# Optimization experiments

Hardware: AMD Instinct MI355X
Metric: run time of the kernel (lower is better)

Reference implementation:

```python
import jax, jax.numpy as jnp
import numpy as np
import math

B, N = 1, 768
C_S, C_Z, C_H, H, P_QK, P_V = 256, 128, 128, 8, 8, 12
EPS, INF, LN_EPS = 1e-8, 1e5, 1e-5


def _quat_to_rot(q):
    # q: [..., 4] normalized quaternion (w, x, y, z) -> [..., 3, 3]
    w, x, y, z = jnp.moveaxis(q, -1, 0)
    r = jnp.stack([
        1 - 2 * (y * y + z * z), 2 * (x * y - w * z), 2 * (x * z + w * y),
        2 * (x * y + w * z), 1 - 2 * (x * x + z * z), 2 * (y * z - w * x),
        2 * (x * z - w * y), 2 * (y * z + w * x), 1 - 2 * (x * x + y * y),
    ], axis=-1)
    return r.reshape(q.shape[:-1] + (3, 3))


def _ln(x, g, b):
    mu = x.mean(-1, keepdims=True)
    var = ((x - mu) ** 2).mean(-1, keepdims=True)
    return (x - mu) * jax.lax.rsqrt(var + LN_EPS) * g + b


def setup_inputs():
    key = jax.random.key(0)
    ks = jax.random.split(key, 20)
    inp = {}
    inp['s'] = jax.random.normal(ks[0], (B, N, C_S), jnp.float32)
    inp['p'] = jax.random.normal(ks[1], (B, N, N, C_Z), jnp.float32)
    q = jax.random.normal(ks[2], (B, N, 4), jnp.float32)
    inp['rot'] = _quat_to_rot(q / jnp.linalg.norm(q, axis=-1, keepdims=True))
    inp['trans'] = 10.0 * jax.random.normal(ks[3], (B, N, 3), jnp.float32)
    inp['mask'] = jnp.ones((B, N), jnp.float32)
    concat_dim = H * C_H + H * P_V * 4 + H * C_Z
    dims = {'q': (H * C_H, C_S), 'kv': (2 * H * C_H, C_S), 'qp': (H * P_QK * 3, C_S),
            'kvp': (H * (P_QK + P_V) * 3, C_S), 'pb': (H, C_Z), 'o': (C_S, concat_dim),
            't1': (C_S, C_S), 't2': (C_S, C_S), 't3': (C_S, C_S), 'bb': (6, C_S)}
    i = 4
    for nm, (do, di) in dims.items():
        k1, k2 = jax.random.split(ks[i]); i += 1
        inp['W' + nm] = 0.02 * jax.random.normal(k1, (do, di), jnp.float32)
        inp['b' + nm] = 0.02 * jax.random.normal(k2, (do,), jnp.float32)
    inp['head_w'] = 0.1 * jax.random.normal(ks[i], (H,), jnp.float32)
    inp['g1'] = jnp.ones((C_S,), jnp.float32)
    inp['be1'] = jnp.zeros((C_S,), jnp.float32)
    inp['g2'] = jnp.ones((C_S,), jnp.float32)
    inp['be2'] = jnp.zeros((C_S,), jnp.float32)
    return inp


def reference(s, p, rot, trans, mask, Wq, bq, Wkv, bkv, Wqp, bqp, Wkvp, bkvp,
              Wpb, bpb, Wo, bo, Wt1, bt1, Wt2, bt2, Wt3, bt3, Wbb, bbb,
              head_w, g1, be1, g2, be2):
    # ---------------- Invariant Point Attention ----------------
    q = (s @ Wq.T + bq).reshape(B, N, H, C_H)
    kv = (s @ Wkv.T + bkv).reshape(B, N, H, 2 * C_H)
    k, v = kv[..., :C_H], kv[..., C_H:]
    # points: linear output is coordinate-major (x-block, y-block, z-block)
    qp = (s @ Wqp.T + bqp).reshape(B, N, 3, H, P_QK)
    qp = jnp.einsum('bnij,bnjhp->bnhpi', rot, qp) + trans[:, :, None, None, :]
    kvp = (s @ Wkvp.T + bkvp).reshape(B, N, 3, H, P_QK + P_V)
    kvp = jnp.einsum('bnij,bnjhp->bnhpi', rot, kvp) + trans[:, :, None, None, :]
    kp, vp = kvp[..., :P_QK, :], kvp[..., P_QK:, :]
    bias_p = p @ Wpb.T + bpb  # [B,N,N,H]
    a = jnp.einsum('bihc,bjhc->bhij', q, k) * math.sqrt(1.0 / (3 * C_H))
    a = a + math.sqrt(1.0 / 3) * jnp.transpose(bias_p, (0, 3, 1, 2))
    d2 = ((qp[:, :, None] - kp[:, None]) ** 2).sum(-1)  # [B,N,N,H,Pqk]
    hw = jax.nn.softplus(head_w) * math.sqrt(1.0 / (3 * (P_QK * 9.0 / 2)))
    pt_att = -0.5 * (d2 * hw[None, None, None, :, None]).sum(-1)  # [B,N,N,H]
    m2 = mask[:, :, None] * mask[:, None, :]
    a = a + jnp.transpose(pt_att, (0, 3, 1, 2)) + (INF * (m2 - 1.0))[:, None]
    att = jax.nn.softmax(a, axis=-1)  # [B,H,N,N]
    o = jnp.einsum('bhij,bjhc->bihc', att, v).reshape(B, N, H * C_H)
    opt = jnp.einsum('bhij,bjhpx->bihpx', att, vp)  # [B,N,H,Pv,3] global
    opt = jnp.einsum('bnji,bnhpj->bnhpi', rot, opt - trans[:, :, None, None, :])
    opt_norm = jnp.sqrt((opt ** 2).sum(-1) + EPS).reshape(B, N, H * P_V)
    opt_flat = jnp.moveaxis(opt.reshape(B, N, H * P_V, 3), -1, -2).reshape(B, N, 3 * H * P_V)
    opair = jnp.einsum('bhij,bijz->bihz', att, p).reshape(B, N, H * C_Z)
    ipa_out = jnp.concatenate([o, opt_flat, opt_norm, opair], -1) @ Wo.T + bo
    # residual + dropout(eval: identity) + LayerNorm
    s1 = _ln(s + ipa_out, g1, be1)
    # ---------------- StructureTransition (1 layer) ----------------
    x = jax.nn.relu(s1 @ Wt1.T + bt1)
    x = jax.nn.relu(x @ Wt2.T + bt2)
    s2 = _ln(s1 + (x @ Wt3.T + bt3), g2, be2)
    # ---------------- BackboneUpdate + masked quaternion compose ----------------
    upd = (s2 @ Wbb.T + bbb) * mask[..., None]  # [B,N,6]
    qvec = jnp.concatenate([jnp.ones(upd.shape[:-1] + (1,), upd.dtype), upd[..., :3]], -1)
    qvec = qvec / jnp.linalg.norm(qvec, axis=-1, keepdims=True)
    rot_new = jnp.einsum('bnij,bnjk->bnik', rot, _quat_to_rot(qvec))
    trans_new = trans + jnp.einsum('bnij,bnj->bni', rot, upd[..., 3:])
    return (s2, rot_new, trans_new)
```

## Files before the change

kernel.cpp:

```cpp
#include <hip/hip_runtime.h>
#include <hip/hip_bf16.h>
#include <math.h>

#define NN 768
#define CS 256
#define CZ 128
#define CH 128
#define HH 8
#define PQK 8
#define PV 12
#define CONCAT 2432
#define ATT_HSTRIDE (768*768)

typedef __bf16 v8bf __attribute__((ext_vector_type(8)));
typedef __bf16 v4bf __attribute__((ext_vector_type(4)));
typedef float  v4f  __attribute__((ext_vector_type(4)));

__device__ inline unsigned short f2bf(float f) {
    union { float f; unsigned u; } v; v.f = f;
    unsigned r = v.u + 0x7FFFu + ((v.u >> 16) & 1u);
    return (unsigned short)(r >> 16);
}
__device__ inline float bf2f(unsigned short u) {
    union { unsigned u; float f; } v; v.u = ((unsigned)u) << 16; return v.f;
}
__device__ inline unsigned encf(float f) {
    unsigned u = __float_as_uint(f);
    return (u >> 31) ? ~u : (u | 0x80000000u);
}
__device__ inline float decf(unsigned e) {
    unsigned u = (e >> 31) ? (e & 0x7FFFFFFFu) : ~e;
    return __uint_as_float(u);
}
__device__ inline v8bf cvt8(const float* p) {
    float4 a = *(const float4*)p;
    float4 b = *(const float4*)(p + 4);
    v8bf v;
    v[0] = (__bf16)a.x; v[1] = (__bf16)a.y; v[2] = (__bf16)a.z; v[3] = (__bf16)a.w;
    v[4] = (__bf16)b.x; v[5] = (__bf16)b.y; v[6] = (__bf16)b.z; v[7] = (__bf16)b.w;
    return v;
}

struct ProjDesc {
    const float* W[4];
    const float* bias[4];
    unsigned short* dstb[4];
    float* dstf[4];
    int D[4];
    int ldc[4];
    int mode[4];
    int blk_start[5];
};

__global__ __launch_bounds__(256) void proj_all(const float* __restrict__ S, ProjDesc d)
{
    __shared__ unsigned short As[64][40];
    __shared__ unsigned short Ws[64][40];
    int bx = blockIdx.x;
    int seg = 0;
    #pragma unroll
    for (int q = 0; q < 3; q++) if (bx >= d.blk_start[q + 1]) seg = q + 1;
    int bd = (bx - d.blk_start[seg]) * 64;
    int bi = blockIdx.y * 64;
    const float* W = d.W[seg];
    int D = d.D[seg], ldc = d.ldc[seg];

    int tid = threadIdx.x, lane = tid & 63, wid = tid >> 6;
    int wr = (wid >> 1) * 32, wc = (wid & 1) * 32;
    v4f acc[2][2] = {};
    int lrow = tid >> 2, lcol = (tid & 3) * 8;
    const float* Ap = S + (size_t)(bi + lrow) * 256 + lcol;
    const float* Wp = W + (size_t)(bd + lrow) * 256 + lcol;
    bool wv = (bd + lrow) < D;
    int fr = lane & 15, fc = (lane >> 4) * 8;

    for (int k0 = 0; k0 < 256; k0 += 32) {
        *(v8bf*)&As[lrow][lcol] = cvt8(Ap + k0);
        v8bf wz = {};
        *(v8bf*)&Ws[lrow][lcol] = wv ? cvt8(Wp + k0) : wz;
        __syncthreads();
        v8bf a0 = *(const v8bf*)&As[wr + fr][fc];
        v8bf a1 = *(const v8bf*)&As[wr + 16 + fr][fc];
        v8bf b0 = *(const v8bf*)&Ws[wc + fr][fc];
        v8bf b1 = *(const v8bf*)&Ws[wc + 16 + fr][fc];
        acc[0][0] = __builtin_amdgcn_mfma_f32_16x16x32_bf16(a0, b0, acc[0][0], 0, 0, 0);
        acc[0][1] = __builtin_amdgcn_mfma_f32_16x16x32_bf16(a0, b1, acc[0][1], 0, 0, 0);
        acc[1][0] = __builtin_amdgcn_mfma_f32_16x16x32_bf16(a1, b0, acc[1][0], 0, 0, 0);
        acc[1][1] = __builtin_amdgcn_mfma_f32_16x16x32_bf16(a1, b1, acc[1][1], 0, 0, 0);
        __syncthreads();
    }
    const float* bias = d.bias[seg];
    int mode = d.mode[seg];
    unsigned short* Cb = d.dstb[seg];
    float* Cf = d.dstf[seg];
    int mrow = (lane >> 4) * 4;
    #pragma unroll
    for (int mi = 0; mi < 2; mi++) {
        #pragma unroll
        for (int ni = 0; ni < 2; ni++) {
            int dd = bd + wc + ni * 16 + fr;
            if (dd < D) {
                #pragma unroll
                for (int r = 0; r < 4; r++) {
                    int m = bi + wr + mi * 16 + mrow + r;
                    float v = acc[mi][ni][r] + bias[dd];
                    if (mode == 2) Cb[(size_t)m * ldc + dd] = f2bf(v);
                    else           Cf[(size_t)m * ldc + dd] = v;
                }
            }
        }
    }
}

__global__ __launch_bounds__(256) void wo_gemm(
    const unsigned short* __restrict__ A,
    const float* __restrict__ W,
    float* __restrict__ C)
{
    __shared__ unsigned short As[64][40];
    __shared__ unsigned short Ws[64][40];
    const int K = 2432, D = 256, ldc = 256;
    int tid = threadIdx.x;
    int bi = blockIdx.y * 64;
    int bd = blockIdx.x * 64;
    int kpb = K / 4;
    int k0b = blockIdx.z * kpb;
    int lane = tid & 63;
    int wid = tid >> 6;
    int wr = (wid >> 1) * 32, wc = (wid & 1) * 32;
    v4f acc[2][2] = {};
    int lrow = tid >> 2;
    int lcol = (tid & 3) * 8;
    const unsigned short* Ap = A + (size_t)(bi + lrow) * K + lcol;
    const float* Wp = W + (size_t)(bd + lrow) * K + lcol;
    int fr = lane & 15, fc = (lane >> 4) * 8;

    for (int k0 = k0b; k0 < k0b + kpb; k0 += 32) {
        *(int4*)&As[lrow][lcol] = *(const int4*)(Ap + k0);
        *(v8bf*)&Ws[lrow][lcol] = cvt8(Wp + k0);
        __syncthreads();
        v8bf a0 = *(const v8bf*)&As[wr + fr][fc];
        v8bf a1 = *(const v8bf*)&As[wr + 16 + fr][fc];
        v8bf b0 = *(const v8bf*)&Ws[wc + fr][fc];
        v8bf b1 = *(const v8bf*)&Ws[wc + 16 + fr][fc];
        acc[0][0] = __builtin_amdgcn_mfma_f32_16x16x32_bf16(a0, b0, acc[0][0], 0, 0, 0);
        acc[0][1] = __builtin_amdgcn_mfma_f32_16x16x32_bf16(a0, b1, acc[0][1], 0, 0, 0);
        acc[1][0] = __builtin_amdgcn_mfma_f32_16x16x32_bf16(a1, b0, acc[1][0], 0, 0, 0);
        acc[1][1] = __builtin_amdgcn_mfma_f32_16x16x32_bf16(a1, b1, acc[1][1], 0, 0, 0);
        __syncthreads();
    }
    int mrow = (lane >> 4) * 4;
    #pragma unroll
    for (int mi = 0; mi < 2; mi++) {
        #pragma unroll
        for (int ni = 0; ni < 2; ni++) {
            int d = bd + wc + ni * 16 + fr;
            #pragma unroll
            for (int r = 0; r < 4; r++) {
                int m = bi + wr + mi * 16 + mrow + r;
                atomicAdd(&C[(size_t)m * ldc + d], acc[mi][ni][r]);
            }
        }
    }
}

__global__ __launch_bounds__(256) void prep2_kernel(
    const float* __restrict__ qpraw, const float* __restrict__ kvpraw,
    const float* __restrict__ rot, const float* __restrict__ trans,
    const unsigned short* __restrict__ kv_bf,
    unsigned short* __restrict__ qph, unsigned short* __restrict__ qpl,
    unsigned short* __restrict__ kph, unsigned short* __restrict__ kpl,
    unsigned short* __restrict__ Vc)
{
    __shared__ unsigned short tile[32][136];
    int bx = blockIdx.x;
    int t = threadIdx.x;
    if (bx < 672) {
        int id = bx*256 + t;
        int i = id / (HH*28);
        int rem = id % (HH*28);
        int h = rem / 28;
        int idx = rem % 28;
        const float* R = rot + i*9;
        const float* T = trans + i*3;
        float s0, s1, s2;
        if (idx < 8) {
            s0 = qpraw[i*192 +   0 + h*8 + idx];
            s1 = qpraw[i*192 +  64 + h*8 + idx];
            s2 = qpraw[i*192 + 128 + h*8 + idx];
        } else {
            int pp = idx - 8;
            s0 = kvpraw[i*480 +   0 + h*20 + pp];
            s1 = kvpraw[i*480 + 160 + h*20 + pp];
            s2 = kvpraw[i*480 + 320 + h*20 + pp];
        }
        float ov[3];
        ov[0] = R[0]*s0 + R[1]*s1 + R[2]*s2 + T[0];
        ov[1] = R[3]*s0 + R[4]*s1 + R[5]*s2 + T[1];
        ov[2] = R[6]*s0 + R[7]*s1 + R[8]*s2 + T[2];
        if (idx < 8) {
            #pragma unroll
            for (int x = 0; x < 3; x++) {
                unsigned short hi = f2bf(ov[x]);
                qph[i*256 + h*32 + idx*3 + x] = hi;
                qpl[i*256 + h*32 + idx*3 + x] = f2bf(ov[x] - bf2f(hi));
            }
            if (idx == 0) {
                #pragma unroll
                for (int m = 24; m < 32; m++) { qph[i*256+h*32+m] = 0; qpl[i*256+h*32+m] = 0; }
            }
        } else if (idx < 16) {
            int pp = idx - 8;
            #pragma unroll
            for (int x = 0; x < 3; x++) {
                unsigned short hi = f2bf(ov[x]);
                kph[i*256 + h*32 + pp*3 + x] = hi;
                kpl[i*256 + h*32 + pp*3 + x] = f2bf(ov[x] - bf2f(hi));
            }
            if (idx == 8) {
                #pragma unroll
                for (int m = 24; m < 32; m++) { kph[i*256+h*32+m] = 0; kpl[i*256+h*32+m] = 0; }
            }
        } else {
            int ppv = idx - 16;
            #pragma unroll
            for (int x = 0; x < 3; x++)
                Vc[((size_t)h*192 + 128 + ppv*3 + x)*768 + i] = f2bf(ov[x]);
        }
    } else {
        int bx2 = bx - 672;
        int h = bx2 & 7, jt = bx2 >> 3;
        int r = t >> 3, c0 = (t & 7) * 16;
        const unsigned short* src = kv_bf + (size_t)(jt*32 + r)*2048 + h*256 + 128 + c0;
        *(int4*)&tile[r][c0]     = *(const int4*)src;
        *(int4*)&tile[r][c0 + 8] = *(const int4*)(src + 8);
        __syncthreads();
        int c = t >> 1, jh = (t & 1) * 16;
        unsigned short tmp[16];
        #pragma unroll
        for (int k = 0; k < 16; k++) tmp[k] = tile[jh + k][c];
        unsigned short* dst = Vc + ((size_t)h*192 + c)*768 + jt*32 + jh;
        *(int4*)dst       = *(int4*)&tmp[0];
        *(int4*)(dst + 8) = *(int4*)&tmp[8];
    }
}

__global__ __launch_bounds__(256) void logits_mfma(
    const unsigned short* __restrict__ q_bf, const unsigned short* __restrict__ kv_bf,
    const unsigned short* __restrict__ qph, const unsigned short* __restrict__ qpl,
    const unsigned short* __restrict__ kph, const unsigned short* __restrict__ kpl,
    const float* __restrict__ mask, const float* __restrict__ head_w,
    float* __restrict__ att, unsigned* __restrict__ m0enc)
{
    __shared__ unsigned short Qs[64][136];
    __shared__ unsigned short Ks[64][136];
    __shared__ float Mi[64], Mj[64];
    int h = blockIdx.z;
    int i0 = blockIdx.y * 64, j0 = blockIdx.x * 64;
    int tid = threadIdx.x, lane = tid & 63, wid = tid >> 6;
    int wr = (wid >> 1) * 32, wc = (wid & 1) * 32;
    int r = tid >> 2, cq = (tid & 3) * 32;
    const unsigned short* qg = q_bf  + (size_t)(i0 + r)*1024 + h*128 + cq;
    const unsigned short* kg = kv_bf + (size_t)(j0 + r)*2048 + h*256 + cq;
    #pragma unroll
    for (int kk = 0; kk < 4; kk++) {
        *(int4*)&Qs[r][cq + kk*8] = *(const int4*)(qg + kk*8);
        *(int4*)&Ks[r][cq + kk*8] = *(const int4*)(kg + kk*8);
    }
    if (tid < 64) {
        Mi[tid] = mask[i0 + tid];
        Mj[tid] = mask[j0 + tid];
    }
    int fr = lane & 15, fc = (lane >> 4) * 8;
    v8bf ah0 = *(const v8bf*)&qph[(size_t)(i0 + wr + fr)*256 + h*32 + fc];
    v8bf ah1 = *(const v8bf*)&qph[(size_t)(i0 + wr + 16 + fr)*256 + h*32 + fc];
    v8bf al0 = *(const v8bf*)&qpl[(size_t)(i0 + wr + fr)*256 + h*32 + fc];
    v8bf al1 = *(const v8bf*)&qpl[(size_t)(i0 + wr + 16 + fr)*256 + h*32 + fc];
    v8bf bh0 = *(const v8bf*)&kph[(size_t)(j0 + wc + fr)*256 + h*32 + fc];
    v8bf bh1 = *(const v8bf*)&kph[(size_t)(j0 + wc + 16 + fr)*256 + h*32 + fc];
    v8bf bl0 = *(const v8bf*)&kpl[(size_t)(j0 + wc + fr)*256 + h*32 + fc];
    v8bf bl1 = *(const v8bf*)&kpl[(size_t)(j0 + wc + 16 + fr)*256 + h*32 + fc];
    float q2a = 0.f, q2b = 0.f, k2a = 0.f, k2b = 0.f;
    #pragma unroll
    for (int m = 0; m < 8; m++) {
        float va = (float)ah0[m] + (float)al0[m];
        float vb = (float)ah1[m] + (float)al1[m];
        float wa = (float)bh0[m] + (float)bl0[m];
        float wb = (float)bh1[m] + (float)bl1[m];
        q2a += va*va; q2b += vb*vb; k2a += wa*wa; k2b += wb*wb;
    }
    q2a += __shfl_xor(q2a, 16); q2a += __shfl_xor(q2a, 32);
    q2b += __shfl_xor(q2b, 16); q2b += __shfl_xor(q2b, 32);
    k2a += __shfl_xor(k2a, 16); k2a += __shfl_xor(k2a, 32);
    k2b += __shfl_xor(k2b, 16); k2b += __shfl_xor(k2b, 32);

    v4f ap[2][2] = {};
    ap[0][0] = __builtin_amdgcn_mfma_f32_16x16x32_bf16(ah0, bh0, ap[0][0], 0, 0, 0);
    ap[0][1] = __builtin_amdgcn_mfma_f32_16x16x32_bf16(ah0, bh1, ap[0][1], 0, 0, 0);
    ap[1][0] = __builtin_amdgcn_mfma_f32_16x16x32_bf16(ah1, bh0, ap[1][0], 0, 0, 0);
    ap[1][1] = __builtin_amdgcn_mfma_f32_16x16x32_bf16(ah1, bh1, ap[1][1], 0, 0, 0);
    ap[0][0] = __builtin_amdgcn_mfma_f32_16x16x32_bf16(ah0, bl0, ap[0][0], 0, 0, 0);
    ap[0][1] = __builtin_amdgcn_mfma_f32_16x16x32_bf16(ah0, bl1, ap[0][1], 0, 0, 0);
    ap[1][0] = __builtin_amdgcn_mfma_f32_16x16x32_bf16(ah1, bl0, ap[1][0], 0, 0, 0);
    ap[1][1] = __builtin_amdgcn_mfma_f32_16x16x32_bf16(ah1, bl1, ap[1][1], 0, 0, 0);
    ap[0][0] = __builtin_amdgcn_mfma_f32_16x16x32_bf16(al0, bh0, ap[0][0], 0, 0, 0);
    ap[0][1] = __builtin_amdgcn_mfma_f32_16x16x32_bf16(al0, bh1, ap[0][1], 0, 0, 0);
    ap[1][0] = __builtin_amdgcn_mfma_f32_16x16x32_bf16(al1, bh0, ap[1][0], 0, 0, 0);
    ap[1][1] = __builtin_amdgcn_mfma_f32_16x16x32_bf16(al1, bh1, ap[1][1], 0, 0, 0);

    __syncthreads();
    v4f aqk[2][2] = {};
    #pragma unroll
    for (int ks = 0; ks < 4; ks++) {
        v8bf a0 = *(const v8bf*)&Qs[wr + fr][ks*32 + fc];
        v8bf a1 = *(const v8bf*)&Qs[wr + 16 + fr][ks*32 + fc];
        v8bf b0 = *(const v8bf*)&Ks[wc + fr][ks*32 + fc];
        v8bf b1 = *(const v8bf*)&Ks[wc + 16 + fr][ks*32 + fc];
        aqk[0][0] = __builtin_amdgcn_mfma_f32_16x16x32_bf16(a0, b0, aqk[0][0], 0, 0, 0);
        aqk[0][1] = __builtin_amdgcn_mfma_f32_16x16x32_bf16(a0, b1, aqk[0][1], 0, 0, 0);
        aqk[1][0] = __builtin_amdgcn_mfma_f32_16x16x32_bf16(a1, b0, aqk[1][0], 0, 0, 0);
        aqk[1][1] = __builtin_amdgcn_mfma_f32_16x16x32_bf16(a1, b1, aqk[1][1], 0, 0, 0);
    }
    float hx = head_w[h];
    float sp = (hx > 20.f) ? hx : log1pf(__expf(hx));
    float hw = sp * 0.09622504486493764f;
    const float scale_qk = 0.05103103630798288f;
    int mrow = (lane >> 4) * 4;
    float val[2][2][4];
    #pragma unroll
    for (int mi = 0; mi < 2; mi++) {
        #pragma unroll
        for (int rr = 0; rr < 4; rr++) {
            float qss = __shfl((mi == 0) ? q2a : q2b, mrow + rr);
            #pragma unroll
            for (int ni = 0; ni < 2; ni++) {
                int jl = wc + ni*16 + fr;
                int il = wr + mi*16 + mrow + rr;
                float kss = (ni == 0) ? k2a : k2b;
                float v = aqk[mi][ni][rr]*scale_qk + hw*ap[mi][ni][rr]
                        - 0.5f*hw*(qss + kss)
                        + 100000.0f*(Mi[il]*Mj[jl] - 1.0f);
                val[mi][ni][rr] = v;
                att[(size_t)h*ATT_HSTRIDE + (size_t)(i0 + il)*768 + (j0 + jl)] = v;
            }
        }
    }
    #pragma unroll
    for (int mi = 0; mi < 2; mi++) {
        #pragma unroll
        for (int rr = 0; rr < 4; rr++) {
            float m = fmaxf(val[mi][0][rr], val[mi][1][rr]);
            #pragma unroll
            for (int d2 = 1; d2 < 16; d2 <<= 1) m = fmaxf(m, __shfl_xor(m, d2));
            if (fr == 0) {
                int il = wr + mi*16 + mrow + rr;
                atomicMax(&m0enc[h*768 + i0 + il], encf(m));
            }
        }
    }
}

__global__ __launch_bounds__(256) void fused_p4_kernel(
    const float* __restrict__ att0,
    const float* __restrict__ p,
    const float* __restrict__ Wpb, const float* __restrict__ bpb,
    const unsigned* __restrict__ m0enc,
    unsigned short* __restrict__ att_bf,
    float* __restrict__ lpart,
    float* __restrict__ opart)
{
    __shared__ unsigned short ptile[2][64][132];
    __shared__ unsigned short wt[16][72];
    __shared__ float bpb_s[8], m8[8], lsum_w[4][8];

    int i = blockIdx.x;
    int quarter = blockIdx.y;
    int jbase = quarter * 192;
    int tid = threadIdx.x, lane = tid & 63, wid = tid >> 6;
    int fr = lane & 15, fc = (lane >> 4) * 8;
    int mrow = (lane >> 4) * 4;

    for (int idx = tid; idx < 16*72; idx += 256) ((unsigned short*)wt)[idx] = 0;
    if (tid < 8) {
        bpb_s[tid] = bpb[tid];
        m8[tid] = decf(m0enc[tid*768 + i]);
    }

    v8bf aW[4];
    #pragma unroll
    for (int ks = 0; ks < 4; ks++) {
        v8bf v = {};
        if (fr < 8) v = cvt8(Wpb + fr*128 + ks*32 + fc);
        aW[ks] = v;
    }

    const float* pbase = p + (size_t)i*98304 + (size_t)jbase*128;
    int ldrow = tid >> 4, ldz = (tid & 15) * 8;
    float4 pfA[4], pfB[4];
    #pragma unroll
    for (int r2 = 0; r2 < 4; r2++) {
        const float* src = pbase + (size_t)(r2*16 + ldrow)*128 + ldz;
        pfA[r2] = *(const float4*)src;
        pfB[r2] = *(const float4*)(src + 4);
    }
    #pragma unroll
    for (int r2 = 0; r2 < 4; r2++) {
        v4bf lo, hi;
        lo[0] = (__bf16)pfA[r2].x; lo[1] = (__bf16)pfA[r2].y;
        lo[2] = (__bf16)pfA[r2].z; lo[3] = (__bf16)pfA[r2].w;
        hi[0] = (__bf16)pfB[r2].x; hi[1] = (__bf16)pfB[r2].y;
        hi[2] = (__bf16)pfB[r2].z; hi[3] = (__bf16)pfB[r2].w;
        *(v4bf*)&ptile[0][r2*16 + ldrow][ldz]     = lo;
        *(v4bf*)&ptile[0][r2*16 + ldrow][ldz + 4] = hi;
    }
    #pragma unroll
    for (int r2 = 0; r2 < 4; r2++) {
        const float* src = pbase + (size_t)(64 + r2*16 + ldrow)*128 + ldz;
        pfA[r2] = *(const float4*)src;
        pfB[r2] = *(const float4*)(src + 4);
    }
    __syncthreads();
    float m0l[4];
    #pragma unroll
    for (int r2 = 0; r2 < 4; r2++) m0l[r2] = (mrow == 0) ? m8[r2] : m8[4 + r2];

    v4f accD[2] = {};
    float lacc[4] = {0.f, 0.f, 0.f, 0.f};
    const float sqrt13 = 0.57735026918962576f;
    bool expo = (mrow < 8);

    for (int t64 = 0; t64 < 3; t64++) {
        int cur = t64 & 1;
        int j0 = jbase + t64 * 64;

        v4f bd = {};
        #pragma unroll
        for (int ks = 0; ks < 4; ks++) {
            int c = ks*32 + fc;
            v4bf blo = *(const v4bf*)&ptile[cur][16*wid + fr][c];
            v4bf bhi = *(const v4bf*)&ptile[cur][16*wid + fr][c + 4];
            v8bf b;
            b[0]=blo[0]; b[1]=blo[1]; b[2]=blo[2]; b[3]=blo[3];
            b[4]=bhi[0]; b[5]=bhi[1]; b[6]=bhi[2]; b[7]=bhi[3];
            bd = __builtin_amdgcn_mfma_f32_16x16x32_bf16(aW[ks], b, bd, 0, 0, 0);
        }
        if (expo) {
            int j = 16*wid + fr;
            float a0v[4], w8[4];
            #pragma unroll
            for (int r2 = 0; r2 < 4; r2++)
                a0v[r2] = att0[((size_t)(mrow + r2)*768 + i)*768 + j0 + j];
            #pragma unroll
            for (int r2 = 0; r2 < 4; r2++) {
                int h = mrow + r2;
                float L = a0v[r2] + sqrt13*(bd[r2] + bpb_s[h]);
                w8[r2] = __expf(fminf(L - m0l[r2], 60.f));
            }
            #pragma unroll
            for (int r2 = 0; r2 < 4; r2++) {
                int h = mrow + r2;
                unsigned short wb = f2bf(w8[r2]);
                wt[h][j] = wb;
                att_bf[((size_t)h*768 + i)*768 + j0 + j] = wb;
            }
            #pragma unroll
            for (int m = 1; m < 16; m <<= 1) {
                #pragma unroll
                for (int r2 = 0; r2 < 4; r2++) w8[r2] += __shfl_xor(w8[r2], m);
            }
            #pragma unroll
            for (int r2 = 0; r2 < 4; r2++) lacc[r2] += w8[r2];
        }
        if (t64 < 2) {
            #pragma unroll
            for (int r2 = 0; r2 < 4; r2++) {
                v4bf lo, hi;
                lo[0] = (__bf16)pfA[r2].x; lo[1] = (__bf16)pfA[r2].y;
                lo[2] = (__bf16)pfA[r2].z; lo[3] = (__bf16)pfA[r2].w;
                hi[0] = (__bf16)pfB[r2].x; hi[1] = (__bf16)pfB[r2].y;
                hi[2] = (__bf16)pfB[r2].z; hi[3] = (__bf16)pfB[r2].w;
                *(v4bf*)&ptile[cur ^ 1][r2*16 + ldrow][ldz]     = lo;
                *(v4bf*)&ptile[cur ^ 1][r2*16 + ldrow][ldz + 4] = hi;
            }
            if (t64 < 1) {
                #pragma unroll
                for (int r2 = 0; r2 < 4; r2++) {
                    const float* src = pbase + (size_t)((t64+2)*64 + r2*16 + ldrow)*128 + ldz;
                    pfA[r2] = *(const float4*)src;
                    pfB[r2] = *(const float4*)(src + 4);
                }
            }
        }
        __syncthreads();

        #pragma unroll
        for (int mm = 0; mm < 2; mm++) {
            int zcol = (2*wid + mm)*16 + fr;
            #pragma unroll
            for (int ks = 0; ks < 2; ks++) {
                v8bf b;
                #pragma unroll
                for (int kk = 0; kk < 8; kk++)
                    b[kk] = *(const __bf16*)&ptile[cur][ks*32 + fc + kk][zcol];
                v8bf a = *(const v8bf*)&wt[fr][ks*32 + fc];
                accD[mm] = __builtin_amdgcn_mfma_f32_16x16x32_bf16(a, b, accD[mm], 0, 0, 0);
            }
        }
        __syncthreads();
    }

    if (fr == 0 && expo) {
        #pragma unroll
        for (int r2 = 0; r2 < 4; r2++) lsum_w[wid][mrow + r2] = lacc[r2];
    }
    __syncthreads();
    if (tid < 8) {
        lpart[(size_t)(quarter*8 + tid)*768 + i] =
            lsum_w[0][tid] + lsum_w[1][tid] + lsum_w[2][tid] + lsum_w[3][tid];
    }
    if (expo) {
        float* ob = opart + (size_t)(quarter*768 + i)*1024;
        #pragma unroll
        for (int mm = 0; mm < 2; mm++) {
            int z = (2*wid + mm)*16 + fr;
            #pragma unroll
            for (int r2 = 0; r2 < 4; r2++)
                ob[(mrow + r2)*128 + z] = accD[mm][r2];
        }
    }
}

__global__ __launch_bounds__(256) void attvc2_mfma(
    const unsigned short* __restrict__ att_bf, const unsigned short* __restrict__ Vc,
    const float* __restrict__ lpart, const float* __restrict__ opart,
    const float* __restrict__ rot, const float* __restrict__ trans,
    unsigned short* __restrict__ concat)
{
    __shared__ unsigned short As[64][72];
    __shared__ unsigned short Bs[64][72];
    int h = blockIdx.z;
    int i0 = blockIdx.y * 64;
    int tid = threadIdx.x, lane = tid & 63, wid = tid >> 6;

    if (blockIdx.x == 3) {
        __shared__ float inv_s2[8][8];
        int t = tid;
        if (t < 64) {
            int k = t >> 3, hh = t & 7;
            int i = i0 + h*8 + k;
            float l = 0.f;
            #pragma unroll
            for (int q = 0; q < 4; q++) l += lpart[(size_t)(q*8 + hh)*768 + i];
            inv_s2[k][hh] = 1.0f / l;
        }
        __syncthreads();
        #pragma unroll
        for (int k = 0; k < 8; k++) {
            int i = i0 + h*8 + k;
            const float* o0 = opart + (size_t)i*1024;
            #pragma unroll
            for (int rep = 0; rep < 4; rep++) {
                int c = t + rep*256;
                float s = o0[c] + o0[(size_t)768*1024 + c]
                        + o0[(size_t)2*768*1024 + c] + o0[(size_t)3*768*1024 + c];
                concat[(size_t)i*CONCAT + 1408 + c] = f2bf(s * inv_s2[k][c >> 7]);
            }
        }
        return;
    }

    int nd0 = blockIdx.x * 64;
    int wr = (wid >> 1) * 32, wc = (wid & 1) * 32;
    int r = tid >> 2, c8 = (tid & 3) * 16;
    int fr = lane & 15, fc = (lane >> 4) * 8;
    v4f acc[2][2] = {};
    for (int k0 = 0; k0 < 768; k0 += 64) {
        const unsigned short* ag = att_bf + ((size_t)h*768 + i0 + r)*768 + k0 + c8;
        const unsigned short* bg = Vc + ((size_t)h*192 + nd0 + r)*768 + k0 + c8;
        *(int4*)&As[r][c8]     = *(const int4*)ag;
        *(int4*)&As[r][c8 + 8] = *(const int4*)(ag + 8);
        *(int4*)&Bs[r][c8]     = *(const int4*)bg;
        *(int4*)&Bs[r][c8 + 8] = *(const int4*)(bg + 8);
        __syncthreads();
        #pragma unroll
        for (int ks = 0; ks < 2; ks++) {
            v8bf a0 = *(const v8bf*)&As[wr + fr][ks*32 + fc];
            v8bf a1 = *(const v8bf*)&As[wr + 16 + fr][ks*32 + fc];
            v8bf b0 = *(const v8bf*)&Bs[wc + fr][ks*32 + fc];
            v8bf b1 = *(const v8bf*)&Bs[wc + 16 + fr][ks*32 + fc];
            acc[0][0] = __builtin_amdgcn_mfma_f32_16x16x32_bf16(a0, b0, acc[0][0], 0, 0, 0);
            acc[0][1] = __builtin_amdgcn_mfma_f32_16x16x32_bf16(a0, b1, acc[0][1], 0, 0, 0);
            acc[1][0] = __builtin_amdgcn_mfma_f32_16x16x32_bf16(a1, b0, acc[1][0], 0, 0, 0);
            acc[1][1] = __builtin_amdgcn_mfma_f32_16x16x32_bf16(a1, b1, acc[1][1], 0, 0, 0);
        }
        __syncthreads();
    }
    int mrow = (lane >> 4) * 4;
    float lv[2][4];
    #pragma unroll
    for (int mi = 0; mi < 2; mi++) {
        int ibase = i0 + wr + mi*16 + mrow;
        #pragma unroll
        for (int rr = 0; rr < 4; rr++) {
            float l = 0.f;
            #pragma unroll
            for (int q = 0; q < 4; q++) l += lpart[(size_t)(q*8 + h)*768 + ibase + rr];
            lv[mi][rr] = 1.0f / l;
        }
    }
    if (nd0 < 128) {
        #pragma unroll
        for (int mi = 0; mi < 2; mi++) {
            #pragma unroll
            for (int ni = 0; ni < 2; ni++) {
                int d = nd0 + wc + ni*16 + fr;
                #pragma unroll
                for (int rr = 0; rr < 4; rr++) {
                    int i = i0 + wr + mi*16 + mrow + rr;
                    concat[(size_t)i*CONCAT + h*128 + d] = f2bf(acc[mi][ni][rr] * lv[mi][rr]);
                }
            }
        }
    } else {
        float* opt_s = (float*)&As[0][0];
        #pragma unroll
        for (int mi = 0; mi < 2; mi++) {
            #pragma unroll
            for (int ni = 0; ni < 2; ni++) {
                int c = wc + ni*16 + fr;
                if (c < 36) {
                    #pragma unroll
                    for (int rr = 0; rr < 4; rr++) {
                        int rl = wr + mi*16 + mrow + rr;
                        opt_s[rl*36 + c] = acc[mi][ni][rr] * lv[mi][rr];
                    }
                }
            }
        }
        __syncthreads();
        for (int it = tid; it < 768; it += 256) {
            int rl = it / 12, pp = it % 12;
            int i = i0 + rl;
            const float* R = rot + i*9;
            const float* T = trans + i*3;
            float y0 = opt_s[rl*36 + pp*3 + 0] - T[0];
            float y1 = opt_s[rl*36 + pp*3 + 1] - T[1];
            float y2 = opt_s[rl*36 + pp*3 + 2] - T[2];
            float o0 = R[0]*y0 + R[3]*y1 + R[6]*y2;
            float o1 = R[1]*y0 + R[4]*y1 + R[7]*y2;
            float o2 = R[2]*y0 + R[5]*y1 + R[8]*y2;
            float nrm = sqrtf(o0*o0 + o1*o1 + o2*o2 + 1e-8f);
            int hp = h*12 + pp;
            unsigned short* cb = concat + (size_t)i*CONCAT;
            cb[1024 +   0 + hp] = f2bf(o0);
            cb[1024 +  96 + hp] = f2bf(o1);
            cb[1024 + 192 + hp] = f2bf(o2);
            cb[1312 + hp] = f2bf(nrm);
        }
    }
}

__global__ __launch_bounds__(256) void tail_kernel(
    const float* __restrict__ s, const float* __restrict__ ipa,
    const float* __restrict__ bo,
    const float* __restrict__ g1, const float* __restrict__ be1,
    const float* __restrict__ Wt1, const float* __restrict__ bt1,
    const float* __restrict__ Wt2, const float* __restrict__ bt2,
    const float* __restrict__ Wt3, const float* __restrict__ bt3,
    const float* __restrict__ g2, const float* __restrict__ be2,
    const float* __restrict__ Wbb, const float* __restrict__ bbb,
    const float* __restrict__ mask,
    const float* __restrict__ rot, const float* __restrict__ trans,
    float* __restrict__ out, float* __restrict__ rot_out, float* __restrict__ trans_out)
{
    __shared__ float s1f[32][257];
    __shared__ unsigned short Ab[32][264];
    __shared__ float upd_s[32][6];
    int i0 = blockIdx.x * 32;
    int tid = threadIdx.x, lane = tid & 63, wid = tid >> 6;
    int fr = lane & 15, fc = (lane >> 4) * 8, mrow = (lane >> 4) * 4;

    int r = tid >> 3, cg = (tid & 7) * 32;
    {
        float xv[32];
        float sum = 0.f, sq = 0.f;
        #pragma unroll
        for (int q = 0; q < 8; q++) {
            float4 a = *(const float4*)&s[(size_t)(i0 + r)*256 + cg + q*4];
            float4 b = *(const float4*)&ipa[(size_t)(i0 + r)*256 + cg + q*4];
            float4 c = *(const float4*)&bo[cg + q*4];
            float v0 = a.x + b.x + c.x, v1 = a.y + b.y + c.y;
            float v2 = a.z + b.z + c.z, v3 = a.w + b.w + c.w;
            xv[q*4+0] = v0; xv[q*4+1] = v1; xv[q*4+2] = v2; xv[q*4+3] = v3;
            sum += v0 + v1 + v2 + v3;
            sq  += v0*v0 + v1*v1 + v2*v2 + v3*v3;
        }
        #pragma unroll
        for (int d = 1; d < 8; d <<= 1) { sum += __shfl_xor(sum, d); sq += __shfl_xor(sq, d); }
        float mu = sum * (1.0f/256.0f);
        float var = sq * (1.0f/256.0f) - mu*mu;
        float rsig = 1.0f / sqrtf(var + 1e-5f);
        #pragma unroll
        for (int c = 0; c < 32; c++) {
            float o = (xv[c] - mu) * rsig * g1[cg + c] + be1[cg + c];
            s1f[r][cg + c] = o;
            Ab[r][cg + c] = f2bf(o);
        }
    }
    __syncthreads();

    const float* Ws[3] = {Wt1, Wt2, Wt3};
    const float* Bs[3] = {bt1, bt2, bt3};
    #pragma unroll
    for (int stage = 0; stage < 3; stage++) {
        const float* W = Ws[stage];
        const float* bias = Bs[stage];
        v4f acc[2][4] = {};
        #pragma unroll
        for (int k0 = 0; k0 < 8; k0++) {
            v8bf a0 = *(const v8bf*)&Ab[fr][k0*32 + fc];
            v8bf a1 = *(const v8bf*)&Ab[16 + fr][k0*32 + fc];
            #pragma unroll
            for (int n = 0; n < 4; n++) {
                int d = wid*64 + n*16 + fr;
                v8bf b = cvt8(&W[(size_t)d*256 + k0*32 + fc]);
                acc[0][n] = __builtin_amdgcn_mfma_f32_16x16x32_bf16(a0, b, acc[0][n], 0, 0, 0);
                acc[1][n] = __builtin_amdgcn_mfma_f32_16x16x32_bf16(a1, b, acc[1][n], 0, 0, 0);
            }
        }
        __syncthreads();
        if (stage < 2) {
            #pragma unroll
            for (int mi = 0; mi < 2; mi++) {
                #pragma unroll
                for (int n = 0; n < 4; n++) {
                    int d = wid*64 + n*16 + fr;
                    #pragma unroll
                    for (int rr = 0; rr < 4; rr++) {
                        int m = mi*16 + mrow + rr;
                        Ab[m][d] = f2bf(fmaxf(acc[mi][n][rr] + bias[d], 0.f));
                    }
                }
            }
        } else {
            #pragma unroll
            for (int mi = 0; mi < 2; mi++) {
                #pragma unroll
                for (int n = 0; n < 4; n++) {
                    int d = wid*64 + n*16 + fr;
                    #pragma unroll
                    for (int rr = 0; rr < 4; rr++) {
                        int m = mi*16 + mrow + rr;
                        s1f[m][d] += acc[mi][n][rr] + bias[d];
                    }
                }
            }
        }
        __syncthreads();
    }

    {
        float xv[32];
        float sum = 0.f, sq = 0.f;
        #pragma unroll
        for (int c = 0; c < 32; c++) {
            float v = s1f[r][cg + c];
            xv[c] = v; sum += v; sq += v*v;
        }
        #pragma unroll
        for (int d = 1; d < 8; d <<= 1) { sum += __shfl_xor(sum, d); sq += __shfl_xor(sq, d); }
        float mu = sum * (1.0f/256.0f);
        float var = sq * (1.0f/256.0f) - mu*mu;
        float rsig = 1.0f / sqrtf(var + 1e-5f);
        float o4[32];
        #pragma unroll
        for (int c = 0; c < 32; c++)
            o4[c] = (xv[c] - mu) * rsig * g2[cg + c] + be2[cg + c];
        #pragma unroll
        for (int q = 0; q < 8; q++) {
            float4 w; w.x = o4[q*4]; w.y = o4[q*4+1]; w.z = o4[q*4+2]; w.w = o4[q*4+3];
            *(float4*)&out[(size_t)(i0 + r)*256 + cg + q*4] = w;
        }
        __syncthreads();
        #pragma unroll
        for (int c = 0; c < 32; c++) s1f[r][cg + c] = o4[c];
    }
    __syncthreads();

    if (tid < 192) {
        int rr = tid / 6, d = tid % 6;
        float acc = bbb[d];
        const float* wb = Wbb + d*256;
        #pragma unroll 8
        for (int c = 0; c < 256; c++) acc += s1f[rr][c] * wb[c];
        upd_s[rr][d] = acc * mask[i0 + rr];
    }
    __syncthreads();

    if (tid < 32) {
        int i = i0 + tid;
        float u0 = upd_s[tid][0], u1 = upd_s[tid][1], u2 = upd_s[tid][2];
        float t0 = upd_s[tid][3], t1 = upd_s[tid][4], t2 = upd_s[tid][5];
        float n = sqrtf(1.f + u0*u0 + u1*u1 + u2*u2);
        float w = 1.f/n, x = u0/n, y = u1/n, z = u2/n;
        float R[3][3];
        R[0][0] = 1.f - 2.f*(y*y + z*z); R[0][1] = 2.f*(x*y - w*z);       R[0][2] = 2.f*(x*z + w*y);
        R[1][0] = 2.f*(x*y + w*z);       R[1][1] = 1.f - 2.f*(x*x + z*z); R[1][2] = 2.f*(y*z - w*x);
        R[2][0] = 2.f*(x*z - w*y);       R[2][1] = 2.f*(y*z + w*x);       R[2][2] = 1.f - 2.f*(x*x + y*y);
        const float* Ri = rot + i*9;
        #pragma unroll
        for (int a = 0; a < 3; a++) {
            #pragma unroll
            for (int b = 0; b < 3; b++) {
                float acc = 0.f;
                #pragma unroll
                for (int j = 0; j < 3; j++) acc += Ri[a*3+j]*R[j][b];
                rot_out[i*9 + a*3 + b] = acc;
            }
            trans_out[i*3 + a] = trans[i*3 + a] + Ri[a*3+0]*t0 + Ri[a*3+1]*t1 + Ri[a*3+2]*t2;
        }
    }
}

extern "C" void kernel_launch(void* const* d_in, const int* in_sizes, int n_in,
                              void* d_out, int out_size, void* d_ws, size_t ws_size,
                              hipStream_t stream)
{
    const float* s      = (const float*)d_in[0];
    const float* p      = (const float*)d_in[1];
    const float* rot    = (const float*)d_in[2];
    const float* trans  = (const float*)d_in[3];
    const float* mask   = (const float*)d_in[4];
    const float* Wq     = (const float*)d_in[5];
    const float* bq     = (const float*)d_in[6];
    const float* Wkv    = (const float*)d_in[7];
    const float* bkv    = (const float*)d_in[8];
    const float* Wqp    = (const float*)d_in[9];
    const float* bqp    = (const float*)d_in[10];
    const float* Wkvp   = (const float*)d_in[11];
    const float* bkvp   = (const float*)d_in[12];
    const float* Wpb    = (const float*)d_in[13];
    const float* bpb    = (const float*)d_in[14];
    const float* Wo     = (const float*)d_in[15];
    const float* bo     = (const float*)d_in[16];
    const float* Wt1    = (const float*)d_in[17];
    const float* bt1    = (const float*)d_in[18];
    const float* Wt2    = (const float*)d_in[19];
    const float* bt2    = (const float*)d_in[20];
    const float* Wt3    = (const float*)d_in[21];
    const float* bt3    = (const float*)d_in[22];
    const float* Wbb    = (const float*)d_in[23];
    const float* bbb    = (const float*)d_in[24];
    const float* head_w = (const float*)d_in[25];
    const float* g1     = (const float*)d_in[26];
    const float* be1    = (const float*)d_in[27];
    const float* g2     = (const float*)d_in[28];
    const float* be2    = (const float*)d_in[29];

    float* out = (float*)d_out;
    char*  wsb = (char*)d_ws;

    size_t off = 0;
    auto alloc = [&](size_t bytes) -> char* {
        char* ptr = wsb + off;
        off += (bytes + 255) & ~(size_t)255;
        return ptr;
    };
    float* qpraw   = (float*)alloc((size_t)NN*192*4);
    float* kvpraw  = (float*)alloc((size_t)NN*480*4);
    float* att     = (float*)alloc((size_t)8*768*768*4);
    float* ipa     = (float*)alloc((size_t)NN*256*4);
    float* lpart   = (float*)alloc((size_t)32*768*4);
    float* opart   = (float*)alloc((size_t)4*768*1024*4);
    unsigned* m0enc = (unsigned*)alloc((size_t)8*768*4);
    unsigned short* q_bf    = (unsigned short*)alloc((size_t)NN*1024*2);
    unsigned short* kv_bf   = (unsigned short*)alloc((size_t)NN*2048*2);
    unsigned short* qph     = (unsigned short*)alloc((size_t)NN*256*2);
    unsigned short* qpl     = (unsigned short*)alloc((size_t)NN*256*2);
    unsigned short* kph     = (unsigned short*)alloc((size_t)NN*256*2);
    unsigned short* kpl     = (unsigned short*)alloc((size_t)NN*256*2);
    unsigned short* Vc      = (unsigned short*)alloc((size_t)8*192*768*2);
    unsigned short* att_bf  = (unsigned short*)alloc((size_t)8*768*768*2);
    unsigned short* concat  = (unsigned short*)alloc((size_t)NN*CONCAT*2);

    hipMemsetAsync(ipa, 0, (size_t)NN*256*4, stream);
    hipMemsetAsync(m0enc, 0, (size_t)8*768*4, stream);

    ProjDesc pd;
    pd.W[0] = Wq;   pd.bias[0] = bq;   pd.dstb[0] = q_bf;   pd.dstf[0] = nullptr; pd.D[0] = 1024; pd.ldc[0] = 1024; pd.mode[0] = 2;
    pd.W[1] = Wkv;  pd.bias[1] = bkv;  pd.dstb[1] = kv_bf;  pd.dstf[1] = nullptr; pd.D[1] = 2048; pd.ldc[1] = 2048; pd.mode[1] = 2;
    pd.W[2] = Wqp;  pd.bias[2] = bqp;  pd.dstb[2] = nullptr; pd.dstf[2] = qpraw;  pd.D[2] = 192;  pd.ldc[2] = 192;  pd.mode[2] = 0;
    pd.W[3] = Wkvp; pd.bias[3] = bkvp; pd.dstb[3] = nullptr; pd.dstf[3] = kvpraw; pd.D[3] = 480;  pd.ldc[3] = 480;  pd.mode[3] = 0;
    pd.blk_start[0] = 0; pd.blk_start[1] = 16; pd.blk_start[2] = 48; pd.blk_start[3] = 51; pd.blk_start[4] = 59;
    proj_all<<<dim3(59, 12), 256, 0, stream>>>(s, pd);

    prep2_kernel<<<672 + 192, 256, 0, stream>>>(
        qpraw, kvpraw, rot, trans, kv_bf, qph, qpl, kph, kpl, Vc);

    logits_mfma<<<dim3(12, 12, 8), 256, 0, stream>>>(
        q_bf, kv_bf, qph, qpl, kph, kpl, mask, head_w, att, m0enc);

    fused_p4_kernel<<<dim3(768, 4), 256, 0, stream>>>(
        att, p, Wpb, bpb, m0enc, att_bf, lpart, opart);

    attvc2_mfma<<<dim3(4, 12, 8), 256, 0, stream>>>(
        att_bf, Vc, lpart, opart, rot, trans, concat);

    wo_gemm<<<dim3(4,12,4), 256, 0, stream>>>(concat, Wo, ipa);

    tail_kernel<<<24, 256, 0, stream>>>(
        s, ipa, bo, g1, be1, Wt1, bt1, Wt2, bt2, Wt3, bt3,
        g2, be2, Wbb, bbb, mask, rot, trans,
        out, out + (size_t)NN*256, out + (size_t)NN*256 + (size_t)NN*9);
}
```

Measured before the change: 190.7 us.

## Split pair kernel j-range in halves and move partial reduction to separate kernel

The fused pair-bias/attention-pair kernel now splits the j dimension into two halves of 384 instead of four quarters of 192, giving a longer double-buffered loop per block and halving the partial sums written to global memory. The reduction of the partial softmax denominators and pair outputs moves out of the attention-value kernel into a dedicated per-row kernel that also stores inverse denominators. The attention-value kernel then reads those inverses directly. This trades some parallelism in the dominant pair-streaming kernel and adds one extra launch in return for less partial-sum traffic and simpler downstream reduction.

```diff
diff --git a/kernel.cpp b/kernel.cpp
--- a/kernel.cpp
+++ b/kernel.cpp
@@ -119,7 +119,7 @@
 {
     __shared__ unsigned short As[64][40];
     __shared__ unsigned short Ws[64][40];
-    const int K = 2432, D = 256, ldc = 256;
+    const int K = 2432, ldc = 256;
     int tid = threadIdx.x;
     int bi = blockIdx.y * 64;
     int bd = blockIdx.x * 64;
@@ -360,7 +360,7 @@
     }
 }
 
-__global__ __launch_bounds__(256) void fused_p4_kernel(
+__global__ __launch_bounds__(256) void fused_p3s_kernel(
     const float* __restrict__ att0,
     const float* __restrict__ p,
     const float* __restrict__ Wpb, const float* __restrict__ bpb,
@@ -374,8 +374,8 @@
     __shared__ float bpb_s[8], m8[8], lsum_w[4][8];
 
     int i = blockIdx.x;
-    int quarter = blockIdx.y;
-    int jbase = quarter * 192;
+    int half = blockIdx.y;
+    int jbase = half * 384;
     int tid = threadIdx.x, lane = tid & 63, wid = tid >> 6;
     int fr = lane & 15, fc = (lane >> 4) * 8;
     int mrow = (lane >> 4) * 4;
@@ -429,7 +429,7 @@
     const float sqrt13 = 0.57735026918962576f;
     bool expo = (mrow < 8);
 
-    for (int t64 = 0; t64 < 3; t64++) {
+    for (int t64 = 0; t64 < 6; t64++) {
         int cur = t64 & 1;
         int j0 = jbase + t64 * 64;
 
@@ -471,7 +471,7 @@
             #pragma unroll
             for (int r2 = 0; r2 < 4; r2++) lacc[r2] += w8[r2];
         }
-        if (t64 < 2) {
+        if (t64 < 5) {
             #pragma unroll
             for (int r2 = 0; r2 < 4; r2++) {
                 v4bf lo, hi;
@@ -482,7 +482,7 @@
                 *(v4bf*)&ptile[cur ^ 1][r2*16 + ldrow][ldz]     = lo;
                 *(v4bf*)&ptile[cur ^ 1][r2*16 + ldrow][ldz + 4] = hi;
             }
-            if (t64 < 1) {
+            if (t64 < 4) {
                 #pragma unroll
                 for (int r2 = 0; r2 < 4; r2++) {
                     const float* src = pbase + (size_t)((t64+2)*64 + r2*16 + ldrow)*128 + ldz;
@@ -515,11 +515,11 @@
     }
     __syncthreads();
     if (tid < 8) {
-        lpart[(size_t)(quarter*8 + tid)*768 + i] =
+        lpart[(size_t)(half*8 + tid)*768 + i] =
             lsum_w[0][tid] + lsum_w[1][tid] + lsum_w[2][tid] + lsum_w[3][tid];
     }
     if (expo) {
-        float* ob = opart + (size_t)(quarter*768 + i)*1024;
+        float* ob = opart + (size_t)(half*768 + i)*1024;
         #pragma unroll
         for (int mm = 0; mm < 2; mm++) {
             int z = (2*wid + mm)*16 + fr;
@@ -530,46 +530,39 @@
     }
 }
 
-__global__ __launch_bounds__(256) void attvc2_mfma(
+__global__ __launch_bounds__(256) void preduce_kernel(
+    const float* __restrict__ lpart, const float* __restrict__ opart,
+    float* __restrict__ linv, unsigned short* __restrict__ concat)
+{
+    __shared__ float inv_s[8];
+    int i = blockIdx.x, t = threadIdx.x;
+    if (t < 8) {
+        float l = lpart[(size_t)t*768 + i] + lpart[(size_t)(8 + t)*768 + i];
+        float iv = 1.0f / l;
+        inv_s[t] = iv;
+        linv[(size_t)t*768 + i] = iv;
+    }
+    __syncthreads();
+    const float* o0 = opart + (size_t)i*1024;
+    const float* o1 = opart + (size_t)(768 + i)*1024;
+    #pragma unroll
+    for (int k = 0; k < 4; k++) {
+        int c = t + k*256;
+        float s = o0[c] + o1[c];
+        concat[(size_t)i*CONCAT + 1408 + c] = f2bf(s * inv_s[c >> 7]);
+    }
+}
+
+__global__ __launch_bounds__(256) void attvc_mfma(
     const unsigned short* __restrict__ att_bf, const unsigned short* __restrict__ Vc,
-    const float* __restrict__ lpart, const float* __restrict__ opart,
-    const float* __restrict__ rot, const float* __restrict__ trans,
-    unsigned short* __restrict__ concat)
+    const float* __restrict__ linv, const float* __restrict__ rot,
+    const float* __restrict__ trans, unsigned short* __restrict__ concat)
 {
     __shared__ unsigned short As[64][72];
     __shared__ unsigned short Bs[64][72];
     int h = blockIdx.z;
-    int i0 = blockIdx.y * 64;
+    int i0 = blockIdx.y * 64, nd0 = blockIdx.x * 64;
     int tid = threadIdx.x, lane = tid & 63, wid = tid >> 6;
-
-    if (blockIdx.x == 3) {
-        __shared__ float inv_s2[8][8];
-        int t = tid;
-        if (t < 64) {
-            int k = t >> 3, hh = t & 7;
-            int i = i0 + h*8 + k;
-            float l = 0.f;
-            #pragma unroll
-            for (int q = 0; q < 4; q++) l += lpart[(size_t)(q*8 + hh)*768 + i];
-            inv_s2[k][hh] = 1.0f / l;
-        }
-        __syncthreads();
-        #pragma unroll
-        for (int k = 0; k < 8; k++) {
-            int i = i0 + h*8 + k;
-            const float* o0 = opart + (size_t)i*1024;
-            #pragma unroll
-            for (int rep = 0; rep < 4; rep++) {
-                int c = t + rep*256;
-                float s = o0[c] + o0[(size_t)768*1024 + c]
-                        + o0[(size_t)2*768*1024 + c] + o0[(size_t)3*768*1024 + c];
-                concat[(size_t)i*CONCAT + 1408 + c] = f2bf(s * inv_s2[k][c >> 7]);
-            }
-        }
-        return;
-    }
-
-    int nd0 = blockIdx.x * 64;
     int wr = (wid >> 1) * 32, wc = (wid & 1) * 32;
     int r = tid >> 2, c8 = (tid & 3) * 16;
     int fr = lane & 15, fc = (lane >> 4) * 8;
@@ -600,13 +593,8 @@
     #pragma unroll
     for (int mi = 0; mi < 2; mi++) {
         int ibase = i0 + wr + mi*16 + mrow;
-        #pragma unroll
-        for (int rr = 0; rr < 4; rr++) {
-            float l = 0.f;
-            #pragma unroll
-            for (int q = 0; q < 4; q++) l += lpart[(size_t)(q*8 + h)*768 + ibase + rr];
-            lv[mi][rr] = 1.0f / l;
-        }
+        float4 l4 = *(const float4*)&linv[(size_t)h*768 + ibase];
+        lv[mi][0] = l4.x; lv[mi][1] = l4.y; lv[mi][2] = l4.z; lv[mi][3] = l4.w;
     }
     if (nd0 < 128) {
         #pragma unroll
@@ -870,8 +858,9 @@
     float* kvpraw  = (float*)alloc((size_t)NN*480*4);
     float* att     = (float*)alloc((size_t)8*768*768*4);
     float* ipa     = (float*)alloc((size_t)NN*256*4);
-    float* lpart   = (float*)alloc((size_t)32*768*4);
-    float* opart   = (float*)alloc((size_t)4*768*1024*4);
+    float* linv    = (float*)alloc((size_t)8*768*4);
+    float* lpart   = (float*)alloc((size_t)16*768*4);
+    float* opart   = (float*)alloc((size_t)2*768*1024*4);
     unsigned* m0enc = (unsigned*)alloc((size_t)8*768*4);
     unsigned short* q_bf    = (unsigned short*)alloc((size_t)NN*1024*2);
     unsigned short* kv_bf   = (unsigned short*)alloc((size_t)NN*2048*2);
@@ -900,11 +889,11 @@
     logits_mfma<<<dim3(12, 12, 8), 256, 0, stream>>>(
         q_bf, kv_bf, qph, qpl, kph, kpl, mask, head_w, att, m0enc);
 
-    fused_p4_kernel<<<dim3(768, 4), 256, 0, stream>>>(
+    fused_p3s_kernel<<<dim3(768, 2), 256, 0, stream>>>(
         att, p, Wpb, bpb, m0enc, att_bf, lpart, opart);
-
-    attvc2_mfma<<<dim3(4, 12, 8), 256, 0, stream>>>(
-        att_bf, Vc, lpart, opart, rot, trans, concat);
+    preduce_kernel<<<768, 256, 0, stream>>>(lpart, opart, linv, concat);
+
+    attvc_mfma<<<dim3(3, 12, 8), 256, 0, stream>>>(att_bf, Vc, linv, rot, trans, concat);
 
     wo_gemm<<<dim3(4,12,4), 256, 0, stream>>>(concat, Wo, ipa);
 
```

After: 196.2 us. 1.03x slower.
